# Kernel optimization log

Measured on AMD Instinct MI355X. Metric: run time of the kernel, lower is better.

The kernel has to match this reference:

```python
import jax, jax.numpy as jnp
import numpy as np

COMMITMENT_COST = 0.25
EPS_NORM = 1e-12  # F.normalize eps
EPS_LOG = 1e-10


def _l2norm(x):
    # F.normalize(x, dim=-1): x / max(||x||, eps)
    n = jnp.linalg.norm(x, axis=-1, keepdims=True)
    return x / jnp.maximum(n, EPS_NORM)


def setup_inputs() -> dict:
    key = jax.random.key(0)
    k1, k2 = jax.random.split(key)
    f_emb = jax.random.normal(k1, (16, 8192, 256), dtype=jnp.float32)
    W = jax.random.normal(k2, (1024, 256), dtype=jnp.float32)  # embedding.weight, N(0,1) init
    return {"f_emb": f_emb, "W": W}


def reference(f_emb, W):
    K, D = W.shape
    flat = f_emb.reshape(-1, D)                       # [N, D]
    fn = _l2norm(flat)                                # normalized inputs
    en = _l2norm(W)                                   # normalized codebook
    # squared L2 distances between normalized vectors: [N, K]
    distances = (jnp.sum(fn * fn, axis=1, keepdims=True)
                 + jnp.sum(en * en, axis=1)
                 - 2.0 * jnp.matmul(fn, en.T))
    encoding_indices = jnp.argmin(distances, axis=1)  # [N]
    encodings = jax.nn.one_hot(encoding_indices, K, dtype=f_emb.dtype)  # [N, K]
    # one-hot @ W == gather; same math, no dense matmul needed
    quantized = W[encoding_indices].reshape(f_emb.shape)
    qn = _l2norm(quantized)
    xn = _l2norm(f_emb)
    e_latent_loss = jnp.mean((jax.lax.stop_gradient(qn) - xn) ** 2)
    q_latent_loss = jnp.mean((qn - jax.lax.stop_gradient(xn)) ** 2)
    latent_loss = q_latent_loss + COMMITMENT_COST * e_latent_loss
    # straight-through estimator
    quantized_st = xn + jax.lax.stop_gradient(qn - xn)
    avg_probs = jnp.mean(encodings, axis=0)
    perplexity = jnp.exp(-jnp.sum(avg_probs * jnp.log(avg_probs + EPS_LOG)))
    return quantized_st, latent_loss, perplexity, encodings
```

## Files before the change

### kernel.cpp

```cpp
#include <hip/hip_runtime.h>
#include <hip/hip_bf16.h>
#include <stdint.h>

#define NROWS 131072
#define KCODES 1024
#define DDIM 256
#define BM 128
#define BK 32

typedef __attribute__((ext_vector_type(4))) float f32x4;
typedef __attribute__((ext_vector_type(8))) short s16x8;
typedef __attribute__((ext_vector_type(4))) short s16x4;

__device__ __forceinline__ unsigned short f2bf(float f) {
  unsigned int u = __float_as_uint(f);
  u += 0x7FFFu + ((u >> 16) & 1u);
  return (unsigned short)(u >> 16);
}
__device__ __forceinline__ float bf2f(unsigned short h) {
  return __uint_as_float(((unsigned int)h) << 16);
}
__device__ __forceinline__ float wred(float v) {
#pragma unroll
  for (int s = 1; s < 64; s <<= 1) v += __shfl_xor(v, s, 64);
  return v;
}

__global__ __launch_bounds__(256) void prep_w(const float* __restrict__ W,
    float* __restrict__ en, unsigned short* __restrict__ enh,
    unsigned short* __restrict__ enl, float* __restrict__ ensq) {
  int wid = threadIdx.x >> 6, lane = threadIdx.x & 63;
  int k = blockIdx.x * 4 + wid;
  float4 w4 = ((const float4*)(W + (size_t)k * DDIM))[lane];
  float ss = wred(w4.x * w4.x + w4.y * w4.y + w4.z * w4.z + w4.w * w4.w);
  float mx = fmaxf(sqrtf(ss), 1e-12f);
  float4 e4;
  e4.x = w4.x / mx; e4.y = w4.y / mx; e4.z = w4.z / mx; e4.w = w4.w / mx;
  ((float4*)(en + (size_t)k * DDIM))[lane] = e4;
  unsigned short h0 = f2bf(e4.x), h1 = f2bf(e4.y), h2 = f2bf(e4.z), h3 = f2bf(e4.w);
  s16x4 hv = { (short)h0, (short)h1, (short)h2, (short)h3 };
  s16x4 lv = { (short)f2bf(e4.x - bf2f(h0)), (short)f2bf(e4.y - bf2f(h1)),
               (short)f2bf(e4.z - bf2f(h2)), (short)f2bf(e4.w - bf2f(h3)) };
  ((s16x4*)(enh + (size_t)k * DDIM))[lane] = hv;
  ((s16x4*)(enl + (size_t)k * DDIM))[lane] = lv;
  float sq = wred(e4.x * e4.x + e4.y * e4.y + e4.z * e4.z + e4.w * e4.w);
  if (lane == 0) ensq[k] = sq;
}

__global__ __launch_bounds__(256) void prep_f(const float* __restrict__ f,
    unsigned short* __restrict__ fnh, unsigned short* __restrict__ fnl) {
  int wid = threadIdx.x >> 6, lane = threadIdx.x & 63;
  int n = blockIdx.x * 4 + wid;
  float4 v = ((const float4*)(f + (size_t)n * DDIM))[lane];
  float ss = wred(v.x * v.x + v.y * v.y + v.z * v.z + v.w * v.w);
  float mx = fmaxf(sqrtf(ss), 1e-12f);
  float4 e4;
  e4.x = v.x / mx; e4.y = v.y / mx; e4.z = v.z / mx; e4.w = v.w / mx;
  unsigned short h0 = f2bf(e4.x), h1 = f2bf(e4.y), h2 = f2bf(e4.z), h3 = f2bf(e4.w);
  s16x4 hv = { (short)h0, (short)h1, (short)h2, (short)h3 };
  s16x4 lv = { (short)f2bf(e4.x - bf2f(h0)), (short)f2bf(e4.y - bf2f(h1)),
               (short)f2bf(e4.z - bf2f(h2)), (short)f2bf(e4.w - bf2f(h3)) };
  ((s16x4*)(fnh + (size_t)n * DDIM))[lane] = hv;
  ((s16x4*)(fnl + (size_t)n * DDIM))[lane] = lv;
}

__global__ __launch_bounds__(256, 2) void gemm3(
    const unsigned short* __restrict__ fnh, const unsigned short* __restrict__ fnl,
    const unsigned short* __restrict__ enh, const unsigned short* __restrict__ enl,
    const float* __restrict__ ensq, int* __restrict__ idx) {
  __shared__ unsigned short lds[2][4][BM * BK];
  int t = threadIdx.x;
  int bm0 = blockIdx.x * BM;
  int lane = t & 63, wid = t >> 6;
  int wr = wid >> 1, wc = wid & 1;
  int l15 = lane & 15, h4 = lane >> 4;

  float run_d[4][4];
  int run_c[4][4];
#pragma unroll
  for (int m = 0; m < 4; ++m)
#pragma unroll
    for (int j = 0; j < 4; ++j) { run_d[m][j] = 1e30f; run_c[m][j] = 0; }

  auto stage = [&](int buf, int it) {
    int ct = it >> 3, kt = it & 7;
#pragma unroll
    for (int i = 0; i < 2; ++i) {
      int ci = i * 256 + t;
      int row = ci >> 2;
      int kc = (((ci & 3) ^ ((row >> 2) & 3)) << 3);
      int koff = kt * BK + kc;
      unsigned int dstb = (unsigned int)((i * 256 + wid * 64) * 8);
      const unsigned short* sAh = fnh + (size_t)(bm0 + row) * DDIM + koff;
      const unsigned short* sAl = fnl + (size_t)(bm0 + row) * DDIM + koff;
      const unsigned short* sBh = enh + (size_t)(ct * 128 + row) * DDIM + koff;
      const unsigned short* sBl = enl + (size_t)(ct * 128 + row) * DDIM + koff;
      __builtin_amdgcn_global_load_lds(
          (const __attribute__((address_space(1))) unsigned int*)sAh,
          (__attribute__((address_space(3))) unsigned int*)&lds[buf][0][dstb], 16, 0, 0);
      __builtin_amdgcn_global_load_lds(
          (const __attribute__((address_space(1))) unsigned int*)sAl,
          (__attribute__((address_space(3))) unsigned int*)&lds[buf][1][dstb], 16, 0, 0);
      __builtin_amdgcn_global_load_lds(
          (const __attribute__((address_space(1))) unsigned int*)sBh,
          (__attribute__((address_space(3))) unsigned int*)&lds[buf][2][dstb], 16, 0, 0);
      __builtin_amdgcn_global_load_lds(
          (const __attribute__((address_space(1))) unsigned int*)sBl,
          (__attribute__((address_space(3))) unsigned int*)&lds[buf][3][dstb], 16, 0, 0);
    }
  };

  f32x4 acc[4][4] = {};
  stage(0, 0);
  for (int it = 0; it < 64; ++it) {
    __syncthreads();
    if (it < 63) stage((it + 1) & 1, it + 1);
    int buf = it & 1;
    s16x8 ah[4], al[4], bh[4], bl[4];
#pragma unroll
    for (int m = 0; m < 4; ++m) {
      int row = wr * 64 + m * 16 + l15;
      int ro = row * BK + ((h4 ^ ((row >> 2) & 3)) << 3);
      ah[m] = *(const s16x8*)&lds[buf][0][ro];
      al[m] = *(const s16x8*)&lds[buf][1][ro];
    }
#pragma unroll
    for (int n = 0; n < 4; ++n) {
      int row = wc * 64 + n * 16 + l15;
      int ro = row * BK + ((h4 ^ ((row >> 2) & 3)) << 3);
      bh[n] = *(const s16x8*)&lds[buf][2][ro];
      bl[n] = *(const s16x8*)&lds[buf][3][ro];
    }
#pragma unroll
    for (int m = 0; m < 4; ++m)
#pragma unroll
      for (int n = 0; n < 4; ++n) {
        acc[m][n] = __builtin_amdgcn_mfma_f32_16x16x32_bf16(ah[m], bh[n], acc[m][n], 0, 0, 0);
        acc[m][n] = __builtin_amdgcn_mfma_f32_16x16x32_bf16(ah[m], bl[n], acc[m][n], 0, 0, 0);
        acc[m][n] = __builtin_amdgcn_mfma_f32_16x16x32_bf16(al[m], bh[n], acc[m][n], 0, 0, 0);
      }
    if ((it & 7) == 7) {
      int ct = it >> 3;
#pragma unroll
      for (int n = 0; n < 4; ++n) {
        float es = ensq[ct * 128 + wc * 64 + n * 16 + l15];
        int c = ct * 128 + wc * 64 + n * 16 + l15;
#pragma unroll
        for (int m = 0; m < 4; ++m)
#pragma unroll
          for (int j = 0; j < 4; ++j) {
            float d = fmaf(-2.f, acc[m][n][j], es);
            if (d < run_d[m][j]) { run_d[m][j] = d; run_c[m][j] = c; }
            acc[m][n][j] = 0.f;
          }
      }
    }
  }

  float2* red = (float2*)lds;
#pragma unroll
  for (int m = 0; m < 4; ++m)
#pragma unroll
    for (int j = 0; j < 4; ++j) {
      float bd = run_d[m][j];
      int bc = run_c[m][j];
#pragma unroll
      for (int s = 1; s < 16; s <<= 1) {
        float od = __shfl_xor(bd, s, 64);
        int oc = __shfl_xor(bc, s, 64);
        if (od < bd || (od == bd && oc < bc)) { bd = od; bc = oc; }
      }
      if (l15 == 0)
        red[wc * BM + wr * 64 + m * 16 + h4 * 4 + j] = make_float2(bd, __int_as_float(bc));
    }
  __syncthreads();
  if (t < BM) {
    float2 p0 = red[t];
    float2 p1 = red[BM + t];
    int c0 = __float_as_int(p0.y), c1 = __float_as_int(p1.y);
    int c = (p1.x < p0.x || (p1.x == p0.x && c1 < c0)) ? c1 : c0;
    idx[bm0 + t] = c;
  }
}

__global__ __launch_bounds__(256) void outputs_k(const float* __restrict__ f,
    const int* __restrict__ idx, const float* __restrict__ en,
    float* __restrict__ outq, float* __restrict__ enc,
    int* __restrict__ hist, double* __restrict__ lacc) {
  int wid = threadIdx.x >> 6, lane = threadIdx.x & 63;
  int n = blockIdx.x * 4 + wid;
  int id = idx[n];
  float4 fv = ((const float4*)(f + (size_t)n * DDIM))[lane];
  float ss = wred(fv.x * fv.x + fv.y * fv.y + fv.z * fv.z + fv.w * fv.w);
  float mx = fmaxf(sqrtf(ss), 1e-12f);
  float4 ev = ((const float4*)(en + (size_t)id * DDIM))[lane];
  ((float4*)(outq + (size_t)n * DDIM))[lane] = ev;
  float dx = ev.x - fv.x / mx;
  float dy = ev.y - fv.y / mx;
  float dz = ev.z - fv.z / mx;
  float dw = ev.w - fv.w / mx;
  float ls = wred(dx * dx + dy * dy + dz * dz + dw * dw);
  if (lane == 0) {
    atomicAdd(&lacc[blockIdx.x & 255], (double)ls);
    atomicAdd(&hist[id], 1);
    enc[(size_t)n * KCODES + id] = 1.0f;
  }
}

__global__ __launch_bounds__(256) void finalize_k(const int* __restrict__ hist,
    const double* __restrict__ lacc, float* __restrict__ out) {
  __shared__ double sd[256];
  __shared__ double se[256];
  int t = threadIdx.x;
  double e = 0.0;
#pragma unroll
  for (int i = 0; i < 4; ++i) {
    int c = hist[t * 4 + i];
    float p = (float)c * (1.0f / 131072.0f);
    e += (double)(p * logf(p + 1e-10f));
  }
  sd[t] = lacc[t];
  se[t] = e;
  __syncthreads();
  for (int s = 128; s > 0; s >>= 1) {
    if (t < s) { sd[t] += sd[t + s]; se[t] += se[t + s]; }
    __syncthreads();
  }
  if (t == 0) {
    out[33554432] = (float)(1.25 * (sd[0] / ((double)NROWS * (double)DDIM)));
    out[33554433] = expf(-(float)se[0]);
  }
}

extern "C" void kernel_launch(void* const* d_in, const int* in_sizes, int n_in,
                              void* d_out, int out_size, void* d_ws, size_t ws_size,
                              hipStream_t stream) {
  const float* f = (const float*)d_in[0];
  const float* W = (const float*)d_in[1];
  float* out = (float*)d_out;
  char* ws = (char*)d_ws;

  int*    hist = (int*)ws;
  double* lacc = (double*)(ws + 4096);
  float*  ensq = (float*)(ws + 8192);
  float*  en   = (float*)(ws + 12288);
  unsigned short* enh = (unsigned short*)(ws + 12288 + 1048576);
  unsigned short* enl = (unsigned short*)(ws + 12288 + 1048576 + 524288);
  int*    idx  = (int*)(ws + 12288 + 2097152);

  char* ob = (char*)d_out;
  const size_t S = 134217984;
  unsigned short* fnh = (unsigned short*)(ob + S);
  unsigned short* fnl = (unsigned short*)(ob + S + 67108864);
  float* enc = out + 33554434;

  hipMemsetAsync(ws, 0, 8192, stream);
  prep_w<<<KCODES / 4, 256, 0, stream>>>(W, en, enh, enl, ensq);
  prep_f<<<NROWS / 4, 256, 0, stream>>>(f, fnh, fnl);
  gemm3<<<NROWS / BM, 256, 0, stream>>>(fnh, fnl, enh, enl, ensq, idx);
  hipMemsetAsync((void*)enc, 0, 536870912ULL, stream);
  outputs_k<<<NROWS / 4, 256, 0, stream>>>(f, idx, en, out, enc, hist, lacc);
  finalize_k<<<1, 256, 0, stream>>>(hist, lacc, out);
}
```

Measured before the change: 1.042 ms.

## Keep input rows register-resident and stream only codebook tiles through LDS

The distance GEMM now loads each wave's 32 normalized input rows (hi and lo bf16 parts, full 256-dim) into registers once. Only 64-code codebook tiles are streamed through double-buffered LDS, and the block grows to 512 threads covering 256 rows. This removes the repeated LDS staging of the A operand and the cross-wave argmin reduction through shared memory, since each wave now owns whole rows and writes indices directly. In exchange it uses many more VGPRs for the resident A fragments, which may reduce occupancy, and gives less reuse of each B fragment per LDS read.

New measurement: 985.5 us. -5.4%, faster.

```diff
diff --git a/kernel.cpp b/kernel.cpp
--- a/kernel.cpp
+++ b/kernel.cpp
@@ -5,8 +5,9 @@
 #define NROWS 131072
 #define KCODES 1024
 #define DDIM 256
-#define BM 128
-#define BK 32
+#define BM2 256
+#define CT 64
+#define NCT 16
 
 typedef __attribute__((ext_vector_type(4))) float f32x4;
 typedef __attribute__((ext_vector_type(8))) short s16x8;
@@ -64,102 +65,92 @@
   ((s16x4*)(fnl + (size_t)n * DDIM))[lane] = lv;
 }
 
-__global__ __launch_bounds__(256, 2) void gemm3(
+__global__ __launch_bounds__(512, 2) void gemm3(
     const unsigned short* __restrict__ fnh, const unsigned short* __restrict__ fnl,
     const unsigned short* __restrict__ enh, const unsigned short* __restrict__ enl,
     const float* __restrict__ ensq, int* __restrict__ idx) {
-  __shared__ unsigned short lds[2][4][BM * BK];
+  __shared__ unsigned short ldsB[2][2][CT * DDIM];
   int t = threadIdx.x;
-  int bm0 = blockIdx.x * BM;
   int lane = t & 63, wid = t >> 6;
-  int wr = wid >> 1, wc = wid & 1;
   int l15 = lane & 15, h4 = lane >> 4;
-
-  float run_d[4][4];
-  int run_c[4][4];
-#pragma unroll
-  for (int m = 0; m < 4; ++m)
+  int wrow = blockIdx.x * BM2 + wid * 32;
+
+  s16x8 ah[2][8], al[2][8];
+#pragma unroll
+  for (int m = 0; m < 2; ++m) {
+    const unsigned short* rh = fnh + (size_t)(wrow + m * 16 + l15) * DDIM + h4 * 8;
+    const unsigned short* rl = fnl + (size_t)(wrow + m * 16 + l15) * DDIM + h4 * 8;
+#pragma unroll
+    for (int ks = 0; ks < 8; ++ks) {
+      ah[m][ks] = *(const s16x8*)(rh + ks * 32);
+      al[m][ks] = *(const s16x8*)(rl + ks * 32);
+    }
+  }
+
+  auto stageB = [&](int buf, int ct) {
+#pragma unroll
+    for (int i = 0; i < 4; ++i) {
+      int ci = i * 512 + t;
+      int c = ci >> 5;
+      int cc = (ci & 31) ^ (c & 7);
+      const unsigned short* sh = enh + (size_t)(ct * CT + c) * DDIM + cc * 8;
+      const unsigned short* sl = enl + (size_t)(ct * CT + c) * DDIM + cc * 8;
+      unsigned int dst = (unsigned int)((i * 512 + wid * 64) * 8);
+      __builtin_amdgcn_global_load_lds(
+          (const __attribute__((address_space(1))) unsigned int*)sh,
+          (__attribute__((address_space(3))) unsigned int*)&ldsB[buf][0][dst], 16, 0, 0);
+      __builtin_amdgcn_global_load_lds(
+          (const __attribute__((address_space(1))) unsigned int*)sl,
+          (__attribute__((address_space(3))) unsigned int*)&ldsB[buf][1][dst], 16, 0, 0);
+    }
+  };
+
+  float run_d[2][4];
+  int run_c[2][4];
+#pragma unroll
+  for (int m = 0; m < 2; ++m)
 #pragma unroll
     for (int j = 0; j < 4; ++j) { run_d[m][j] = 1e30f; run_c[m][j] = 0; }
 
-  auto stage = [&](int buf, int it) {
-    int ct = it >> 3, kt = it & 7;
-#pragma unroll
-    for (int i = 0; i < 2; ++i) {
-      int ci = i * 256 + t;
-      int row = ci >> 2;
-      int kc = (((ci & 3) ^ ((row >> 2) & 3)) << 3);
-      int koff = kt * BK + kc;
-      unsigned int dstb = (unsigned int)((i * 256 + wid * 64) * 8);
-      const unsigned short* sAh = fnh + (size_t)(bm0 + row) * DDIM + koff;
-      const unsigned short* sAl = fnl + (size_t)(bm0 + row) * DDIM + koff;
-      const unsigned short* sBh = enh + (size_t)(ct * 128 + row) * DDIM + koff;
-      const unsigned short* sBl = enl + (size_t)(ct * 128 + row) * DDIM + koff;
-      __builtin_amdgcn_global_load_lds(
-          (const __attribute__((address_space(1))) unsigned int*)sAh,
-          (__attribute__((address_space(3))) unsigned int*)&lds[buf][0][dstb], 16, 0, 0);
-      __builtin_amdgcn_global_load_lds(
-          (const __attribute__((address_space(1))) unsigned int*)sAl,
-          (__attribute__((address_space(3))) unsigned int*)&lds[buf][1][dstb], 16, 0, 0);
-      __builtin_amdgcn_global_load_lds(
-          (const __attribute__((address_space(1))) unsigned int*)sBh,
-          (__attribute__((address_space(3))) unsigned int*)&lds[buf][2][dstb], 16, 0, 0);
-      __builtin_amdgcn_global_load_lds(
-          (const __attribute__((address_space(1))) unsigned int*)sBl,
-          (__attribute__((address_space(3))) unsigned int*)&lds[buf][3][dstb], 16, 0, 0);
-    }
-  };
-
-  f32x4 acc[4][4] = {};
-  stage(0, 0);
-  for (int it = 0; it < 64; ++it) {
+  f32x4 acc[2][4] = {};
+  stageB(0, 0);
+  for (int ct = 0; ct < NCT; ++ct) {
     __syncthreads();
-    if (it < 63) stage((it + 1) & 1, it + 1);
-    int buf = it & 1;
-    s16x8 ah[4], al[4], bh[4], bl[4];
-#pragma unroll
-    for (int m = 0; m < 4; ++m) {
-      int row = wr * 64 + m * 16 + l15;
-      int ro = row * BK + ((h4 ^ ((row >> 2) & 3)) << 3);
-      ah[m] = *(const s16x8*)&lds[buf][0][ro];
-      al[m] = *(const s16x8*)&lds[buf][1][ro];
+    if (ct < NCT - 1) stageB((ct + 1) & 1, ct + 1);
+    int buf = ct & 1;
+#pragma unroll
+    for (int ks = 0; ks < 8; ++ks) {
+#pragma unroll
+      for (int n = 0; n < 4; ++n) {
+        int X = (ks * 4 + h4) ^ (l15 & 7);
+        const unsigned short* bp = &ldsB[buf][0][(n * 16 + l15) * DDIM + X * 8];
+        s16x8 bh = *(const s16x8*)bp;
+        s16x8 bl = *(const s16x8*)(bp + CT * DDIM);
+        acc[0][n] = __builtin_amdgcn_mfma_f32_16x16x32_bf16(ah[0][ks], bh, acc[0][n], 0, 0, 0);
+        acc[1][n] = __builtin_amdgcn_mfma_f32_16x16x32_bf16(ah[1][ks], bh, acc[1][n], 0, 0, 0);
+        acc[0][n] = __builtin_amdgcn_mfma_f32_16x16x32_bf16(ah[0][ks], bl, acc[0][n], 0, 0, 0);
+        acc[1][n] = __builtin_amdgcn_mfma_f32_16x16x32_bf16(ah[1][ks], bl, acc[1][n], 0, 0, 0);
+        acc[0][n] = __builtin_amdgcn_mfma_f32_16x16x32_bf16(al[0][ks], bh, acc[0][n], 0, 0, 0);
+        acc[1][n] = __builtin_amdgcn_mfma_f32_16x16x32_bf16(al[1][ks], bh, acc[1][n], 0, 0, 0);
+      }
     }
 #pragma unroll
     for (int n = 0; n < 4; ++n) {
-      int row = wc * 64 + n * 16 + l15;
-      int ro = row * BK + ((h4 ^ ((row >> 2) & 3)) << 3);
-      bh[n] = *(const s16x8*)&lds[buf][2][ro];
-      bl[n] = *(const s16x8*)&lds[buf][3][ro];
-    }
-#pragma unroll
-    for (int m = 0; m < 4; ++m)
-#pragma unroll
-      for (int n = 0; n < 4; ++n) {
-        acc[m][n] = __builtin_amdgcn_mfma_f32_16x16x32_bf16(ah[m], bh[n], acc[m][n], 0, 0, 0);
-        acc[m][n] = __builtin_amdgcn_mfma_f32_16x16x32_bf16(ah[m], bl[n], acc[m][n], 0, 0, 0);
-        acc[m][n] = __builtin_amdgcn_mfma_f32_16x16x32_bf16(al[m], bh[n], acc[m][n], 0, 0, 0);
-      }
-    if ((it & 7) == 7) {
-      int ct = it >> 3;
-#pragma unroll
-      for (int n = 0; n < 4; ++n) {
-        float es = ensq[ct * 128 + wc * 64 + n * 16 + l15];
-        int c = ct * 128 + wc * 64 + n * 16 + l15;
-#pragma unroll
-        for (int m = 0; m < 4; ++m)
-#pragma unroll
-          for (int j = 0; j < 4; ++j) {
-            float d = fmaf(-2.f, acc[m][n][j], es);
-            if (d < run_d[m][j]) { run_d[m][j] = d; run_c[m][j] = c; }
-            acc[m][n][j] = 0.f;
-          }
-      }
-    }
-  }
-
-  float2* red = (float2*)lds;
-#pragma unroll
-  for (int m = 0; m < 4; ++m)
+      int c = ct * CT + n * 16 + l15;
+      float es = ensq[c];
+#pragma unroll
+      for (int m = 0; m < 2; ++m)
+#pragma unroll
+        for (int j = 0; j < 4; ++j) {
+          float d = fmaf(-2.f, acc[m][n][j], es);
+          if (d < run_d[m][j]) { run_d[m][j] = d; run_c[m][j] = c; }
+          acc[m][n][j] = 0.f;
+        }
+    }
+  }
+
+#pragma unroll
+  for (int m = 0; m < 2; ++m)
 #pragma unroll
     for (int j = 0; j < 4; ++j) {
       float bd = run_d[m][j];
@@ -170,17 +161,8 @@
         int oc = __shfl_xor(bc, s, 64);
         if (od < bd || (od == bd && oc < bc)) { bd = od; bc = oc; }
       }
-      if (l15 == 0)
-        red[wc * BM + wr * 64 + m * 16 + h4 * 4 + j] = make_float2(bd, __int_as_float(bc));
-    }
-  __syncthreads();
-  if (t < BM) {
-    float2 p0 = red[t];
-    float2 p1 = red[BM + t];
-    int c0 = __float_as_int(p0.y), c1 = __float_as_int(p1.y);
-    int c = (p1.x < p0.x || (p1.x == p0.x && c1 < c0)) ? c1 : c0;
-    idx[bm0 + t] = c;
-  }
+      if (l15 == 0) idx[wrow + m * 16 + h4 * 4 + j] = bc;
+    }
 }
 
 __global__ __launch_bounds__(256) void outputs_k(const float* __restrict__ f,
@@ -257,7 +239,7 @@
   hipMemsetAsync(ws, 0, 8192, stream);
   prep_w<<<KCODES / 4, 256, 0, stream>>>(W, en, enh, enl, ensq);
   prep_f<<<NROWS / 4, 256, 0, stream>>>(f, fnh, fnl);
-  gemm3<<<NROWS / BM, 256, 0, stream>>>(fnh, fnl, enh, enl, ensq, idx);
+  gemm3<<<NROWS / BM2, 512, 0, stream>>>(fnh, fnl, enh, enl, ensq, idx);
   hipMemsetAsync((void*)enc, 0, 536870912ULL, stream);
   outputs_k<<<NROWS / 4, 256, 0, stream>>>(f, idx, en, out, enc, hist, lacc);
   finalize_k<<<1, 256, 0, stream>>>(hist, lacc, out);
```
